# Optimization experiments

Hardware: AMD Instinct MI355X
Metric: run time of the kernel (lower is better)

The kernel has to match this reference:

```python
import jax, jax.numpy as jnp
import numpy as np

N_S, N_G, E = 4000, 50000, 250000   # sample nodes, gene nodes, edges per relation
D, H, C1, C3 = 128, 4, 32, 64       # input dim, heads, layer-1 per-head dim, layer-3 per-head dim
NEG_SLOPE = 0.2


def gatv2(x_src, x_dst, src, dst, ea, Wl, bl, Wr, br, We, att, bias, n_dst, concat):
    """PyG GATv2Conv (add_self_loops=False, edge_dim=1, eval mode)."""
    Hh, C = att.shape
    xl = (x_src @ Wl + bl).reshape(-1, Hh, C)          # [N_src, H, C]
    xr = (x_dst @ Wr + br).reshape(-1, Hh, C)          # [N_dst, H, C]
    ee = (ea @ We).reshape(-1, Hh, C)                  # [E, H, C]
    m = jax.nn.leaky_relu(xl[src] + xr[dst] + ee, NEG_SLOPE)   # [E, H, C]
    logits = jnp.einsum('ehc,hc->eh', m, att)          # [E, H]
    # segment softmax over incoming edges of each destination node
    lmax = jax.ops.segment_max(logits, dst, num_segments=n_dst)[dst]
    ex = jnp.exp(logits - lmax)
    denom = jax.ops.segment_sum(ex, dst, num_segments=n_dst)[dst]
    alpha = ex / denom                                 # [E, H]
    out = jax.ops.segment_sum(xl[src] * alpha[:, :, None], dst, num_segments=n_dst)  # [N_dst, H, C]
    out = out.reshape(n_dst, Hh * C) if concat else out.mean(axis=1)
    return out + bias


def setup_inputs() -> dict:
    key = jax.random.key(0)
    ks = jax.random.split(key, 40)
    p = lambda i, shape: jax.random.normal(ks[i], shape, dtype=jnp.float32) * 0.05
    HC1, HC3 = H * C1, H * C3
    inp = {
        'x_mrna': p(0, (N_S, D)),
        'x_gene': p(1, (N_G, D)),
        'sg_src': jax.random.randint(ks[2], (E,), 0, N_S),
        'sg_dst': jax.random.randint(ks[3], (E,), 0, N_G),
        'gs_src': jax.random.randint(ks[4], (E,), 0, N_G),
        'gs_dst': jax.random.randint(ks[5], (E,), 0, N_S),
        'ea_sg': p(6, (E, 1)),
        'ea_gs': p(7, (E, 1)),
        # layer-1 GATv2 params, relation mrna->gene
        'Wl1_sg': p(8, (D, HC1)), 'bl1_sg': p(9, (HC1,)),
        'Wr1_sg': p(10, (D, HC1)), 'br1_sg': p(11, (HC1,)),
        'We1_sg': p(12, (1, HC1)), 'att1_sg': p(13, (H, C1)), 'bo1_sg': p(14, (HC1,)),
        # layer-1 GATv2 params, relation gene->mrna
        'Wl1_gs': p(15, (D, HC1)), 'bl1_gs': p(16, (HC1,)),
        'Wr1_gs': p(17, (D, HC1)), 'br1_gs': p(18, (HC1,)),
        'We1_gs': p(19, (1, HC1)), 'att1_gs': p(20, (H, C1)), 'bo1_gs': p(21, (HC1,)),
        # layer-3 GATv2 params, relation gene->mrna (concat=False)
        'Wl3_gs': p(22, (HC1, HC3)), 'bl3_gs': p(23, (HC3,)),
        'Wr3_gs': p(24, (HC1, HC3)), 'br3_gs': p(25, (HC3,)),
        'We3_gs': p(26, (1, HC3)), 'att3_gs': p(27, (H, C3)), 'bo3_gs': p(28, (C3,)),
        # self-loop linears for omic ('mrna') nodes
        'Wsl1': p(29, (D, C1)), 'bsl1': p(30, (C1,)),
        'Wsl3': p(31, (HC1, C3)), 'bsl3': p(32, (C3,)),
    }
    return inp


def reference(x_mrna, x_gene, sg_src, sg_dst, gs_src, gs_dst, ea_sg, ea_gs,
              Wl1_sg, bl1_sg, Wr1_sg, br1_sg, We1_sg, att1_sg, bo1_sg,
              Wl1_gs, bl1_gs, Wr1_gs, br1_gs, We1_gs, att1_gs, bo1_gs,
              Wl3_gs, bl3_gs, Wr3_gs, br3_gs, We3_gs, att3_gs, bo3_gs,
              Wsl1, bsl1, Wsl3, bsl3):
    # ---- layer 1 (HeteroConv over both relations) ----
    x1_gene = gatv2(x_mrna, x_gene, sg_src, sg_dst, ea_sg,
                    Wl1_sg, bl1_sg, Wr1_sg, br1_sg, We1_sg, att1_sg, bo1_sg, N_G, True)
    x1_mrna = gatv2(x_gene, x_mrna, gs_src, gs_dst, ea_gs,
                    Wl1_gs, bl1_gs, Wr1_gs, br1_gs, We1_gs, att1_gs, bo1_gs, N_S, True)
    # self-loop linear on omic nodes, repeated across heads (repeat(1, heads))
    x1_mrna = x1_mrna + jnp.tile(x_mrna @ Wsl1 + bsl1, (1, H))
    x1_mrna = jax.nn.relu(x1_mrna)
    x1_gene = jax.nn.relu(x1_gene)
    # ---- three_layers=False: x2 = x1; layer 3 (concat=False, head mean) ----
    x3_mrna = gatv2(x1_gene, x1_mrna, gs_src, gs_dst, ea_gs,
                    Wl3_gs, bl3_gs, Wr3_gs, br3_gs, We3_gs, att3_gs, bo3_gs, N_S, False)
    x3_mrna = x3_mrna + (x1_mrna @ Wsl3 + bsl3)
    x3_mrna = jax.nn.relu(x3_mrna)
    # integrator=None, single omic view -> squeeze to [N_S, C3]
    return x3_mrna
```

## Files before the change

kernel.cpp:

```cpp
#include <hip/hip_runtime.h>
#include <cstdint>
#include <cstddef>

#define NS 4000
#define NG 50000
#define NE 250000
#define DIM 128
#define NDST_TOT (NG + NS)

typedef __bf16 bf16_t;
typedef bf16_t bf16x8 __attribute__((ext_vector_type(8)));
typedef bf16_t bf16x4 __attribute__((ext_vector_type(4)));
typedef bf16_t bf16x2 __attribute__((ext_vector_type(2)));
typedef float floatx4 __attribute__((ext_vector_type(4)));

#define HIST_B 977
#define WT_TOT 143360
#define XM_W 64000
#define XG_W 800000
#define PREP_B 3935
struct HPArgs {
  const int* sgd; const int* gsd;
  int* cnt; unsigned short* rank_sg; unsigned short* rank_gs;
  const float* W[8]; bf16_t* Wt[8]; int N[8]; int e0[8];
  const float* xm; bf16_t* xbm;
  const float* xg; bf16_t* xbg;
};

__global__ __launch_bounds__(256) void histprep(HPArgs a) {
  if (blockIdx.x < HIST_B) {
    int e = blockIdx.x * 256 + threadIdx.x;
    if (e < NE) {
      a.rank_sg[e] = (unsigned short)atomicAdd(a.cnt + a.sgd[e], 1);
      a.rank_gs[e] = (unsigned short)atomicAdd(a.cnt + NG + a.gsd[e], 1);
    }
  } else {
    int u = (blockIdx.x - HIST_B) * 256 + threadIdx.x;
    if (u < WT_TOT) {
      int c = 0;
#pragma unroll
      for (int i = 1; i < 8; i++) if (u >= a.e0[i]) c = i;
      int idx = u - a.e0[c];
      int N = a.N[c];
      int k = idx / N, n = idx - k * N;
      a.Wt[c][n * 128 + k] = (bf16_t)a.W[c][idx];
    } else if (u < WT_TOT + XM_W) {
      int j = (u - WT_TOT) * 8;
      float4 v0 = *reinterpret_cast<const float4*>(a.xm + j);
      float4 v1 = *reinterpret_cast<const float4*>(a.xm + j + 4);
      bf16x8 b;
      b[0] = (bf16_t)v0.x; b[1] = (bf16_t)v0.y; b[2] = (bf16_t)v0.z; b[3] = (bf16_t)v0.w;
      b[4] = (bf16_t)v1.x; b[5] = (bf16_t)v1.y; b[6] = (bf16_t)v1.z; b[7] = (bf16_t)v1.w;
      *reinterpret_cast<bf16x8*>(a.xbm + j) = b;
    } else {
      int j = (u - WT_TOT - XM_W) * 8;
      float4 v0 = *reinterpret_cast<const float4*>(a.xg + j);
      float4 v1 = *reinterpret_cast<const float4*>(a.xg + j + 4);
      bf16x8 b;
      b[0] = (bf16_t)v0.x; b[1] = (bf16_t)v0.y; b[2] = (bf16_t)v0.z; b[3] = (bf16_t)v0.w;
      b[4] = (bf16_t)v1.x; b[5] = (bf16_t)v1.y; b[6] = (bf16_t)v1.z; b[7] = (bf16_t)v1.w;
      *reinterpret_cast<bf16x8*>(a.xbg + j) = b;
    }
  }
}

__global__ __launch_bounds__(1024) void scan_fused(const int* __restrict__ cnt,
                                                   int* __restrict__ rp,
                                                   int* af, int n) {
  __shared__ int wsum[16];
  __shared__ int pfx_s;
  int i = blockIdx.x * 1024 + threadIdx.x;
  int lane = threadIdx.x & 63, w = threadIdx.x >> 6;
  int v = (i < n) ? cnt[i] : 0;
  int x = v;
#pragma unroll
  for (int off = 1; off < 64; off <<= 1) {
    int y = __shfl_up(x, off);
    if (lane >= off) x += y;
  }
  if (lane == 63) wsum[w] = x;
  __syncthreads();
  if (w == 0 && lane < 16) {
    int s = wsum[lane];
#pragma unroll
    for (int off = 1; off < 16; off <<= 1) {
      int y = __shfl_up(s, off);
      if (lane >= off) s += y;
    }
    wsum[lane] = s;
  }
  __syncthreads();
  int incl = x + (w ? wsum[w - 1] : 0);
  if (threadIdx.x == 0) atomicExch(af + blockIdx.x, wsum[15] + 1);
  if (w == 0) {
    int pred = 0;
    if (lane < (int)blockIdx.x) {
      int t;
      while ((t = atomicAdd(af + lane, 0)) == 0) { __builtin_amdgcn_s_sleep(8); }
      pred = t - 1;
    }
#pragma unroll
    for (int off = 32; off > 0; off >>= 1) pred += __shfl_down(pred, off);
    if (lane == 0) pfx_s = pred;
  }
  __syncthreads();
  if (i < n) rp[i] = incl - v + pfx_s;
  if (i == 0) rp[n] = 2 * NE;
}

#define SCAT_HALF 245
#define SCAT_B 490
struct SGArgs {
  const int* sgd; const int* gsd; const int* sgs; const int* gss;
  const float* easg; const float* eags;
  const int* rp; const unsigned short* rank_sg; const unsigned short* rank_gs;
  uint2* meta;
  const bf16_t* X[5];
  const bf16_t* Wt[5];
  const float* Bv[5];
  bf16_t* Y[5];
  int M[5];
  int Ncol[5];
  int blk0[5];
};

__global__ __launch_bounds__(256, 4) void scatgemm(SGArgs a) {
  if (blockIdx.x < SCAT_B) {
    int rel = (int)blockIdx.x >= SCAT_HALF;
    int b = (int)blockIdx.x - (rel ? SCAT_HALF : 0);
    int t4 = (b * 256 + (int)threadIdx.x) * 4;
    if (t4 < NE) {
      const int* dp = rel ? a.gsd : a.sgd;
      const int* sp = rel ? a.gss : a.sgs;
      const float* ep = rel ? a.eags : a.easg;
      const unsigned short* rk = rel ? a.rank_gs : a.rank_sg;
      const int* rpb = a.rp + (rel ? NG : 0);
      int4 d4 = *reinterpret_cast<const int4*>(dp + t4);
      int4 s4 = *reinterpret_cast<const int4*>(sp + t4);
      float4 e4 = *reinterpret_cast<const float4*>(ep + t4);
      ushort4 r4 = *reinterpret_cast<const ushort4*>(rk + t4);
      int p0 = rpb[d4.x] + (int)r4.x;
      int p1 = rpb[d4.y] + (int)r4.y;
      int p2 = rpb[d4.z] + (int)r4.z;
      int p3 = rpb[d4.w] + (int)r4.w;
      uint2 v0, v1, v2, v3;
      v0.x = (unsigned)s4.x; v0.y = __float_as_uint(e4.x);
      v1.x = (unsigned)s4.y; v1.y = __float_as_uint(e4.y);
      v2.x = (unsigned)s4.z; v2.y = __float_as_uint(e4.z);
      v3.x = (unsigned)s4.w; v3.y = __float_as_uint(e4.w);
      a.meta[p0] = v0;
      a.meta[p1] = v1;
      a.meta[p2] = v2;
      a.meta[p3] = v3;
    }
    return;
  }
  int bid = blockIdx.x - SCAT_B;
  int c = 0;
#pragma unroll
  for (int i = 1; i < 5; i++) if (bid >= a.blk0[i]) c = i;
  const bf16_t* X = a.X[c];
  const bf16_t* Wt = a.Wt[c];
  const float* B = a.Bv[c];
  bf16_t* Y = a.Y[c];
  int M = a.M[c];
  int N = a.Ncol[c];

  int wv = threadIdx.x >> 6, lane = threadIdx.x & 63;
  int m16 = lane & 15, quad = lane >> 4;
  int wrow0 = (bid - a.blk0[c]) * 256 + wv * 64;

  bf16x8 afrag[4][4];
#pragma unroll
  for (int rt = 0; rt < 4; rt++) {
    int arow = wrow0 + rt * 16 + m16;
    const bf16_t* xp = X + (size_t)arow * DIM + quad * 8;
#pragma unroll
    for (int kk = 0; kk < 4; kk++) {
      bf16x8 av = {};
      if (arow < M) av = *reinterpret_cast<const bf16x8*>(xp + kk * 32);
      afrag[rt][kk] = av;
    }
  }

  int ncols = N >> 4;
  for (int nt = 0; nt < ncols; nt++) {
    const bf16_t* bptr = Wt + (size_t)(nt * 16 + m16) * DIM + quad * 8;
    bf16x8 bfrag[4];
#pragma unroll
    for (int kk = 0; kk < 4; kk++)
      bfrag[kk] = *reinterpret_cast<const bf16x8*>(bptr + kk * 32);
    float4 bias = *reinterpret_cast<const float4*>(B + nt * 16 + quad * 4);
#pragma unroll
    for (int rt = 0; rt < 4; rt++) {
      floatx4 acc = {0.f, 0.f, 0.f, 0.f};
#pragma unroll
      for (int kk = 0; kk < 4; kk++)
        acc = __builtin_amdgcn_mfma_f32_16x16x32_bf16(bfrag[kk], afrag[rt][kk], acc, 0, 0, 0);
      int row = wrow0 + rt * 16 + m16;
      if (row < M) {
        bf16x4 o;
        o[0] = (bf16_t)(acc[0] + bias.x);
        o[1] = (bf16_t)(acc[1] + bias.y);
        o[2] = (bf16_t)(acc[2] + bias.z);
        o[3] = (bf16_t)(acc[3] + bias.w);
        *reinterpret_cast<bf16x4*>(Y + (size_t)row * N + nt * 16 + quad * 4) = o;
      }
    }
  }
}

template <int NCFG>
struct GArgs {
  const bf16_t* X[NCFG];
  const bf16_t* Wt[NCFG];
  const float* Bv[NCFG];
  bf16_t* Y[NCFG];
  int M[NCFG];
  int Ncol[NCFG];
  int blk0[NCFG];
};

template <int NCFG>
__global__ __launch_bounds__(256, 4) void gemm_multi(GArgs<NCFG> a) {
  int c = 0;
#pragma unroll
  for (int i = 1; i < NCFG; i++) if ((int)blockIdx.x >= a.blk0[i]) c = i;
  const bf16_t* X = a.X[c];
  const bf16_t* Wt = a.Wt[c];
  const float* B = a.Bv[c];
  bf16_t* Y = a.Y[c];
  int M = a.M[c];
  int N = a.Ncol[c];

  int wv = threadIdx.x >> 6, lane = threadIdx.x & 63;
  int m16 = lane & 15, quad = lane >> 4;
  int wrow0 = ((int)blockIdx.x - a.blk0[c]) * 128 + wv * 32;

  bf16x8 afrag[2][4];
#pragma unroll
  for (int rt = 0; rt < 2; rt++) {
    int arow = wrow0 + rt * 16 + m16;
    const bf16_t* xp = X + (size_t)arow * DIM + quad * 8;
#pragma unroll
    for (int kk = 0; kk < 4; kk++) {
      bf16x8 av = {};
      if (arow < M) av = *reinterpret_cast<const bf16x8*>(xp + kk * 32);
      afrag[rt][kk] = av;
    }
  }

  int ncols = N >> 4;
  for (int nt = 0; nt < ncols; nt++) {
    const bf16_t* bptr = Wt + (size_t)(nt * 16 + m16) * DIM + quad * 8;
    bf16x8 bfrag[4];
#pragma unroll
    for (int kk = 0; kk < 4; kk++)
      bfrag[kk] = *reinterpret_cast<const bf16x8*>(bptr + kk * 32);
    float4 bias = *reinterpret_cast<const float4*>(B + nt * 16 + quad * 4);
#pragma unroll
    for (int rt = 0; rt < 2; rt++) {
      floatx4 acc = {0.f, 0.f, 0.f, 0.f};
#pragma unroll
      for (int kk = 0; kk < 4; kk++)
        acc = __builtin_amdgcn_mfma_f32_16x16x32_bf16(bfrag[kk], afrag[rt][kk], acc, 0, 0, 0);
      int row = wrow0 + rt * 16 + m16;
      if (row < M) {
        bf16x4 o;
        o[0] = (bf16_t)(acc[0] + bias.x);
        o[1] = (bf16_t)(acc[1] + bias.y);
        o[2] = (bf16_t)(acc[2] + bias.z);
        o[3] = (bf16_t)(acc[3] + bias.w);
        *reinterpret_cast<bf16x4*>(Y + (size_t)row * N + nt * 16 + quad * 4) = o;
      }
    }
  }
}

#define SGB 3125
__global__ __launch_bounds__(256) void gatC(
    const int* __restrict__ rp, const uint2* __restrict__ meta,
    const float* __restrict__ WeS, const float* __restrict__ attS,
    const float* __restrict__ boS,
    const bf16_t* __restrict__ xlS, const bf16_t* __restrict__ xrS,
    bf16_t* __restrict__ outS,
    const float* __restrict__ WeG, const float* __restrict__ attG,
    const float* __restrict__ boG,
    const bf16_t* __restrict__ xlG, const bf16_t* __restrict__ xrG,
    const bf16_t* __restrict__ slG, bf16_t* __restrict__ outG) {
  __shared__ uint2 smeta[256];
  __shared__ float lacc[16][128];
  __shared__ float lden[16][4];
  int lane = threadIdx.x & 63, wv = threadIdx.x >> 6;
  int gl = lane & 15, grp = lane >> 4;

  if (blockIdx.x < SGB) {
    int wid = blockIdx.x * 4 + wv;
    int d0 = wid * 4;
    int q = lane < 5 ? lane : 0;
    int rv = rp[d0 + q];
    int beg = __shfl(rv, grp), end = __shfl(rv, grp + 1);
    int dst = d0 + grp;

    float wev[8], atv[8], xrv[8], acc[8];
    *reinterpret_cast<float4*>(wev) = *reinterpret_cast<const float4*>(WeS + gl * 8);
    *reinterpret_cast<float4*>(wev + 4) = *reinterpret_cast<const float4*>(WeS + gl * 8 + 4);
    *reinterpret_cast<float4*>(atv) = *reinterpret_cast<const float4*>(attS + gl * 8);
    *reinterpret_cast<float4*>(atv + 4) = *reinterpret_cast<const float4*>(attS + gl * 8 + 4);
    bf16x8 xrb = *reinterpret_cast<const bf16x8*>(xrS + (size_t)dst * 128 + gl * 8);
#pragma unroll
    for (int v = 0; v < 8; v++) { xrv[v] = (float)xrb[v]; acc[v] = 0.f; }
    float den = 0.f;

    for (int i0 = beg; i0 < end; i0 += 16) {
      int cnt = min(16, end - i0);
      int s_l = 0; float ea_l = 0.f;
      if (gl < cnt) {
        uint2 mv = meta[i0 + gl];
        s_l = (int)mv.x; ea_l = __uint_as_float(mv.y);
      }
      int base = lane & 48;
      float ea = __shfl(ea_l, base);
      bf16x8 xlb = *reinterpret_cast<const bf16x8*>(
          xlS + (size_t)__shfl(s_l, base) * 128 + gl * 8);
      for (int k = 0; k < cnt; k++) {
        bf16x8 cur = xlb;
        float eac = ea;
        if (k + 1 < cnt) {
          ea = __shfl(ea_l, base + k + 1);
          xlb = *reinterpret_cast<const bf16x8*>(
              xlS + (size_t)__shfl(s_l, base + k + 1) * 128 + gl * 8);
        }
        float p = 0.f, xf[8];
#pragma unroll
        for (int v = 0; v < 8; v++) {
          xf[v] = (float)cur[v];
          float z = fmaf(eac, wev[v], xrv[v]) + xf[v];
          z = z > 0.f ? z : 0.2f * z;
          p = fmaf(z, atv[v], p);
        }
        p += __shfl_xor(p, 1);
        p += __shfl_xor(p, 2);
        float ex = __expf(p);
        den += ex;
#pragma unroll
        for (int v = 0; v < 8; v++) acc[v] = fmaf(ex, xf[v], acc[v]);
      }
    }
    float inv = den > 0.f ? 1.f / den : 0.f;
    bf16x8 o;
#pragma unroll
    for (int v = 0; v < 8; v++) {
      float val = acc[v] * inv + boS[gl * 8 + v];
      o[v] = (bf16_t)(val > 0.f ? val : 0.f);
    }
    *reinterpret_cast<bf16x8*>(outS + (size_t)dst * 128 + gl * 8) = o;
  } else {
    int d = (int)blockIdx.x - SGB;
    const int* rpg = rp + NG;
    int G = wv * 4 + grp;
    int tid = threadIdx.x;

    float wev[8], atv[8], xrv[8], acc[8];
    *reinterpret_cast<float4*>(wev) = *reinterpret_cast<const float4*>(WeG + gl * 8);
    *reinterpret_cast<float4*>(wev + 4) = *reinterpret_cast<const float4*>(WeG + gl * 8 + 4);
    *reinterpret_cast<float4*>(atv) = *reinterpret_cast<const float4*>(attG + gl * 8);
    *reinterpret_cast<float4*>(atv + 4) = *reinterpret_cast<const float4*>(attG + gl * 8 + 4);
    bf16x8 xrb = *reinterpret_cast<const bf16x8*>(xrG + (size_t)d * 128 + gl * 8);
#pragma unroll
    for (int v = 0; v < 8; v++) { xrv[v] = (float)xrb[v]; acc[v] = 0.f; }
    float den = 0.f;

    int beg = rpg[d], end = rpg[d + 1];
    for (int base = beg; base < end; base += 256) {
      int cntb = min(256, end - base);
      __syncthreads();
      if (tid < cntb) smeta[tid] = meta[base + tid];
      __syncthreads();
      int e = G;
      uint2 mv; bf16x8 xlb;
      if (e < cntb) {
        mv = smeta[e];
        xlb = *reinterpret_cast<const bf16x8*>(xlG + (size_t)mv.x * 128 + gl * 8);
      }
      while (e < cntb) {
        bf16x8 cur = xlb;
        float eac = __uint_as_float(mv.y);
        int en = e + 16;
        if (en < cntb) {
          mv = smeta[en];
          xlb = *reinterpret_cast<const bf16x8*>(xlG + (size_t)mv.x * 128 + gl * 8);
        }
        float p = 0.f, xf[8];
#pragma unroll
        for (int v = 0; v < 8; v++) {
          xf[v] = (float)cur[v];
          float z = fmaf(eac, wev[v], xrv[v]) + xf[v];
          z = z > 0.f ? z : 0.2f * z;
          p = fmaf(z, atv[v], p);
        }
        p += __shfl_xor(p, 1);
        p += __shfl_xor(p, 2);
        float ex = __expf(p);
        den += ex;
#pragma unroll
        for (int v = 0; v < 8; v++) acc[v] = fmaf(ex, xf[v], acc[v]);
        e = en;
      }
    }
#pragma unroll
    for (int v = 0; v < 8; v++) lacc[G][gl * 8 + v] = acc[v];
    if ((gl & 3) == 0) lden[G][gl >> 2] = den;
    __syncthreads();
    if (wv != 0) return;
    int ch = lane * 2;
    int h = lane >> 4;
    float a0 = 0.f, a1 = 0.f, dh = 0.f;
#pragma unroll
    for (int g2 = 0; g2 < 16; g2++) {
      a0 += lacc[g2][ch];
      a1 += lacc[g2][ch + 1];
      dh += lden[g2][h];
    }
    float inv = dh > 0.f ? 1.f / dh : 0.f;
    float v0 = a0 * inv + boG[ch] + (float)slG[(size_t)d * 32 + (ch & 31)];
    float v1 = a1 * inv + boG[ch + 1] + (float)slG[(size_t)d * 32 + ((ch + 1) & 31)];
    bf16x2 o;
    o[0] = (bf16_t)(v0 > 0.f ? v0 : 0.f);
    o[1] = (bf16_t)(v1 > 0.f ? v1 : 0.f);
    *reinterpret_cast<bf16x2*>(outG + (size_t)d * 128 + ch) = o;
  }
}

__global__ __launch_bounds__(256) void gatE(
    const int* __restrict__ rp, const uint2* __restrict__ meta,
    const float* __restrict__ We, const float* __restrict__ att,
    const bf16_t* __restrict__ xl, const bf16_t* __restrict__ xr,
    const float* __restrict__ bo, const bf16_t* __restrict__ sl,
    float* __restrict__ out) {
  __shared__ uint2 smeta[256];
  __shared__ float lacc[16][256];
  __shared__ float lden[16][4];
  int lane = threadIdx.x & 63, wv = threadIdx.x >> 6;
  int gl = lane & 15, grp = lane >> 4;
  int G = wv * 4 + grp;
  int tid = threadIdx.x;
  int d = blockIdx.x;

  float wev[16], atv[16], xrv[16], acc[16];
#pragma unroll
  for (int b = 0; b < 4; b++) {
    *reinterpret_cast<float4*>(wev + b * 4) =
        *reinterpret_cast<const float4*>(We + gl * 16 + b * 4);
    *reinterpret_cast<float4*>(atv + b * 4) =
        *reinterpret_cast<const float4*>(att + gl * 16 + b * 4);
  }
  {
    bf16x8 r0 = *reinterpret_cast<const bf16x8*>(xr + (size_t)d * 256 + gl * 16);
    bf16x8 r1 = *reinterpret_cast<const bf16x8*>(xr + (size_t)d * 256 + gl * 16 + 8);
#pragma unroll
    for (int v = 0; v < 8; v++) { xrv[v] = (float)r0[v]; xrv[v + 8] = (float)r1[v]; }
  }
#pragma unroll
  for (int v = 0; v < 16; v++) acc[v] = 0.f;
  float den = 0.f;

  int beg = rp[d], end = rp[d + 1];
  for (int base = beg; base < end; base += 256) {
    int cntb = min(256, end - base);
    __syncthreads();
    if (tid < cntb) smeta[tid] = meta[base + tid];
    __syncthreads();
    int e = G;
    uint2 mv; bf16x8 x0, x1;
    if (e < cntb) {
      mv = smeta[e];
      x0 = *reinterpret_cast<const bf16x8*>(xl + (size_t)mv.x * 256 + gl * 16);
      x1 = *reinterpret_cast<const bf16x8*>(xl + (size_t)mv.x * 256 + gl * 16 + 8);
    }
    while (e < cntb) {
      bf16x8 c0 = x0, c1 = x1;
      float eac = __uint_as_float(mv.y);
      int en = e + 16;
      if (en < cntb) {
        mv = smeta[en];
        x0 = *reinterpret_cast<const bf16x8*>(xl + (size_t)mv.x * 256 + gl * 16);
        x1 = *reinterpret_cast<const bf16x8*>(xl + (size_t)mv.x * 256 + gl * 16 + 8);
      }
      float p = 0.f, xf[16];
#pragma unroll
      for (int v = 0; v < 8; v++) { xf[v] = (float)c0[v]; xf[v + 8] = (float)c1[v]; }
#pragma unroll
      for (int v = 0; v < 16; v++) {
        float z = fmaf(eac, wev[v], xrv[v]) + xf[v];
        z = z > 0.f ? z : 0.2f * z;
        p = fmaf(z, atv[v], p);
      }
      p += __shfl_xor(p, 1);
      p += __shfl_xor(p, 2);
      float ex = __expf(p);
      den += ex;
#pragma unroll
      for (int v = 0; v < 16; v++) acc[v] = fmaf(ex, xf[v], acc[v]);
      e = en;
    }
  }
#pragma unroll
  for (int v = 0; v < 16; v++) lacc[G][gl * 16 + v] = acc[v];
  if ((gl & 3) == 0) lden[G][gl >> 2] = den;
  __syncthreads();
  if (wv != 0) return;
  int ch = lane * 4;
  int h = lane >> 4;
  float a[4] = {0.f, 0.f, 0.f, 0.f};
  float dh = 0.f;
#pragma unroll
  for (int g2 = 0; g2 < 16; g2++) {
#pragma unroll
    for (int v = 0; v < 4; v++) a[v] += lacc[g2][ch + v];
    dh += lden[g2][h];
  }
  float inv = dh > 0.f ? 1.f / dh : 0.f;
#pragma unroll
  for (int v = 0; v < 4; v++) {
    float s_ = a[v] * inv;
    s_ += __shfl_xor(s_, 16);
    s_ += __shfl_xor(s_, 32);
    if (lane < 16) {
      int c = (lane & 15) * 4 + v;
      float val = 0.25f * s_ + bo[c] + (float)sl[(size_t)d * 64 + c];
      out[(size_t)d * 64 + c] = val > 0.f ? val : 0.f;
    }
  }
}


static inline int nblk(long long threads) { return (int)((threads + 255) / 256); }
static inline int nrow(int M, int R) { return (M + R - 1) / R; }

extern "C" void kernel_launch(void* const* d_in, const int* in_sizes, int n_in,
                              void* d_out, int out_size, void* d_ws, size_t ws_size,
                              hipStream_t stream) {
  const float* x_mrna = (const float*)d_in[0];
  const float* x_gene = (const float*)d_in[1];
  const int* sg_src = (const int*)d_in[2];
  const int* sg_dst = (const int*)d_in[3];
  const int* gs_src = (const int*)d_in[4];
  const int* gs_dst = (const int*)d_in[5];
  const float* ea_sg = (const float*)d_in[6];
  const float* ea_gs = (const float*)d_in[7];
  const float* Wl1_sg = (const float*)d_in[8];
  const float* bl1_sg = (const float*)d_in[9];
  const float* Wr1_sg = (const float*)d_in[10];
  const float* br1_sg = (const float*)d_in[11];
  const float* We1_sg = (const float*)d_in[12];
  const float* att1_sg = (const float*)d_in[13];
  const float* bo1_sg = (const float*)d_in[14];
  const float* Wl1_gs = (const float*)d_in[15];
  const float* bl1_gs = (const float*)d_in[16];
  const float* Wr1_gs = (const float*)d_in[17];
  const float* br1_gs = (const float*)d_in[18];
  const float* We1_gs = (const float*)d_in[19];
  const float* att1_gs = (const float*)d_in[20];
  const float* bo1_gs = (const float*)d_in[21];
  const float* Wl3_gs = (const float*)d_in[22];
  const float* bl3_gs = (const float*)d_in[23];
  const float* Wr3_gs = (const float*)d_in[24];
  const float* br3_gs = (const float*)d_in[25];
  const float* We3_gs = (const float*)d_in[26];
  const float* att3_gs = (const float*)d_in[27];
  const float* bo3_gs = (const float*)d_in[28];
  const float* Wsl1 = (const float*)d_in[29];
  const float* bsl1 = (const float*)d_in[30];
  const float* Wsl3 = (const float*)d_in[31];
  const float* bsl3 = (const float*)d_in[32];

  float* ws = (float*)d_ws;
  bf16_t* xl1_gs = (bf16_t*)(ws + 0);
  bf16_t* xl1_sg = (bf16_t*)(ws + 3200000);
  bf16_t* xr1_sg = (bf16_t*)(ws + 3456000);
  bf16_t* xr1_gs = (bf16_t*)(ws + 6656000);
  bf16_t* xl3    = (bf16_t*)(ws + 0);
  bf16_t* xr3    = (bf16_t*)(ws + 6400000);
  bf16_t* xb_mrna = (bf16_t*)(ws + 6912000);
  bf16_t* xb_gene = (bf16_t*)(ws + 7168000);
  bf16_t* x1_gene = (bf16_t*)(ws + 10368000);
  bf16_t* x1_mrna = (bf16_t*)(ws + 13568000);
  bf16_t* sl1    = (bf16_t*)(ws + 13824000);
  bf16_t* sl3    = (bf16_t*)(ws + 13856000);
  int*   ib      = (int*)(ws + 13920000);
  int* cnt  = ib + 0;
  int* af   = ib + 54000;
  int* rpc  = ib + 54064;
  unsigned short* rank_sg = (unsigned short*)(ib + 108066);
  unsigned short* rank_gs = (unsigned short*)(ib + 233066);
  uint2* meta = (uint2*)(ib + 358066);
  bf16_t* wtb = (bf16_t*)(ib + 1358066);

  bf16_t* wt_l1sg = wtb + 0;
  bf16_t* wt_r1sg = wtb + 16384;
  bf16_t* wt_l1gs = wtb + 32768;
  bf16_t* wt_r1gs = wtb + 49152;
  bf16_t* wt_l3   = wtb + 65536;
  bf16_t* wt_r3   = wtb + 98304;
  bf16_t* wt_sl1  = wtb + 131072;
  bf16_t* wt_sl3  = wtb + 135168;

  hipMemsetAsync(cnt, 0, (54000 + 64) * sizeof(int), stream);

  {
    HPArgs hp;
    hp.sgd = sg_dst; hp.gsd = gs_dst;
    hp.cnt = cnt; hp.rank_sg = rank_sg; hp.rank_gs = rank_gs;
    const float* Wsrc[8] = {Wl1_sg, Wr1_sg, Wl1_gs, Wr1_gs, Wl3_gs, Wr3_gs, Wsl1, Wsl3};
    bf16_t* Wdst[8] = {wt_l1sg, wt_r1sg, wt_l1gs, wt_r1gs, wt_l3, wt_r3, wt_sl1, wt_sl3};
    int Nn[8] = {128, 128, 128, 128, 256, 256, 32, 64};
    int e0[8] = {0, 16384, 32768, 49152, 65536, 98304, 131072, 135168};
    for (int i = 0; i < 8; i++) { hp.W[i] = Wsrc[i]; hp.Wt[i] = Wdst[i]; hp.N[i] = Nn[i]; hp.e0[i] = e0[i]; }
    hp.xm = x_mrna; hp.xbm = xb_mrna;
    hp.xg = x_gene; hp.xbg = xb_gene;
    histprep<<<HIST_B + PREP_B, 256, 0, stream>>>(hp);
  }

  int nchunks = (NDST_TOT + 1023) / 1024;
  scan_fused<<<nchunks, 1024, 0, stream>>>(cnt, rpc, af, NDST_TOT);

  {
    SGArgs sa;
    sa.sgd = sg_dst; sa.gsd = gs_dst; sa.sgs = sg_src; sa.gss = gs_src;
    sa.easg = ea_sg; sa.eags = ea_gs;
    sa.rp = rpc; sa.rank_sg = rank_sg; sa.rank_gs = rank_gs; sa.meta = meta;
    const bf16_t* Xs[5] = {xb_mrna, xb_gene, xb_gene, xb_mrna, xb_mrna};
    const bf16_t* Ws[5] = {wt_l1sg, wt_r1sg, wt_l1gs, wt_r1gs, wt_sl1};
    const float* Bs[5] = {bl1_sg, br1_sg, bl1_gs, br1_gs, bsl1};
    bf16_t* Ys[5] = {xl1_sg, xr1_sg, xl1_gs, xr1_gs, sl1};
    int Ms[5] = {NS, NG, NG, NS, NS};
    int Ns[5] = {128, 128, 128, 128, 32};
    int b0 = 0;
    for (int i = 0; i < 5; i++) {
      sa.X[i] = Xs[i]; sa.Wt[i] = Ws[i]; sa.Bv[i] = Bs[i]; sa.Y[i] = Ys[i];
      sa.M[i] = Ms[i]; sa.Ncol[i] = Ns[i]; sa.blk0[i] = b0;
      b0 += nrow(Ms[i], 256);
    }
    scatgemm<<<SCAT_B + b0, 256, 0, stream>>>(sa);
  }

  gatC<<<SGB + NS, 256, 0, stream>>>(
      rpc, meta,
      We1_sg, att1_sg, bo1_sg, xl1_sg, xr1_sg, x1_gene,
      We1_gs, att1_gs, bo1_gs, xl1_gs, xr1_gs, sl1, x1_mrna);

  {
    GArgs<3> ga;
    const bf16_t* Xs[3] = {x1_gene, x1_mrna, x1_mrna};
    const bf16_t* Ws[3] = {wt_l3, wt_r3, wt_sl3};
    const float* Bs[3] = {bl3_gs, br3_gs, bsl3};
    bf16_t* Ys[3] = {xl3, xr3, sl3};
    int Ms[3] = {NG, NS, NS};
    int Ns[3] = {256, 256, 64};
    int b0 = 0;
    for (int i = 0; i < 3; i++) {
      ga.X[i] = Xs[i]; ga.Wt[i] = Ws[i]; ga.Bv[i] = Bs[i]; ga.Y[i] = Ys[i];
      ga.M[i] = Ms[i]; ga.Ncol[i] = Ns[i]; ga.blk0[i] = b0;
      b0 += nrow(Ms[i], 128);
    }
    gemm_multi<3><<<b0, 256, 0, stream>>>(ga);
  }

  gatE<<<NS, 256, 0, stream>>>(rpc + NG, meta, We3_gs, att3_gs,
                               xl3, xr3, bo3_gs, sl3, (float*)d_out);
}
```

Before: 279.2 us.

## Regroup preprocessing: pair histogram with layer-1 GEMM, run scatter standalone

Restructures the pre-attention pipeline. A standalone prep kernel now does the bf16 conversion and weight transposes. The edge histogram atomics are fused into the layer-1 GEMM launch, placed after the GEMM blocks, and the CSR scatter becomes its own kernel after the scan. The intent is to overlap the atomic-heavy histogram with MFMA GEMM work instead of with the conversion pass. The cost is one extra kernel launch and a scatter that no longer overlaps with anything.

Result: no change. 279.3 us (+0.0%).

```diff
diff --git a/kernel.cpp b/kernel.cpp
--- a/kernel.cpp
+++ b/kernel.cpp
@@ -14,107 +14,50 @@
 typedef bf16_t bf16x2 __attribute__((ext_vector_type(2)));
 typedef float floatx4 __attribute__((ext_vector_type(4)));
 
-#define HIST_B 977
 #define WT_TOT 143360
 #define XM_W 64000
 #define XG_W 800000
 #define PREP_B 3935
-struct HPArgs {
-  const int* sgd; const int* gsd;
-  int* cnt; unsigned short* rank_sg; unsigned short* rank_gs;
+struct PArgs {
   const float* W[8]; bf16_t* Wt[8]; int N[8]; int e0[8];
   const float* xm; bf16_t* xbm;
   const float* xg; bf16_t* xbg;
 };
 
-__global__ __launch_bounds__(256) void histprep(HPArgs a) {
-  if (blockIdx.x < HIST_B) {
-    int e = blockIdx.x * 256 + threadIdx.x;
-    if (e < NE) {
-      a.rank_sg[e] = (unsigned short)atomicAdd(a.cnt + a.sgd[e], 1);
-      a.rank_gs[e] = (unsigned short)atomicAdd(a.cnt + NG + a.gsd[e], 1);
-    }
+__global__ __launch_bounds__(256) void prep(PArgs a) {
+  int u = blockIdx.x * 256 + threadIdx.x;
+  if (u < WT_TOT) {
+    int c = 0;
+#pragma unroll
+    for (int i = 1; i < 8; i++) if (u >= a.e0[i]) c = i;
+    int idx = u - a.e0[c];
+    int N = a.N[c];
+    int k = idx / N, n = idx - k * N;
+    a.Wt[c][n * 128 + k] = (bf16_t)a.W[c][idx];
+  } else if (u < WT_TOT + XM_W) {
+    int j = (u - WT_TOT) * 8;
+    float4 v0 = *reinterpret_cast<const float4*>(a.xm + j);
+    float4 v1 = *reinterpret_cast<const float4*>(a.xm + j + 4);
+    bf16x8 b;
+    b[0] = (bf16_t)v0.x; b[1] = (bf16_t)v0.y; b[2] = (bf16_t)v0.z; b[3] = (bf16_t)v0.w;
+    b[4] = (bf16_t)v1.x; b[5] = (bf16_t)v1.y; b[6] = (bf16_t)v1.z; b[7] = (bf16_t)v1.w;
+    *reinterpret_cast<bf16x8*>(a.xbm + j) = b;
   } else {
-    int u = (blockIdx.x - HIST_B) * 256 + threadIdx.x;
-    if (u < WT_TOT) {
-      int c = 0;
-#pragma unroll
-      for (int i = 1; i < 8; i++) if (u >= a.e0[i]) c = i;
-      int idx = u - a.e0[c];
-      int N = a.N[c];
-      int k = idx / N, n = idx - k * N;
-      a.Wt[c][n * 128 + k] = (bf16_t)a.W[c][idx];
-    } else if (u < WT_TOT + XM_W) {
-      int j = (u - WT_TOT) * 8;
-      float4 v0 = *reinterpret_cast<const float4*>(a.xm + j);
-      float4 v1 = *reinterpret_cast<const float4*>(a.xm + j + 4);
-      bf16x8 b;
-      b[0] = (bf16_t)v0.x; b[1] = (bf16_t)v0.y; b[2] = (bf16_t)v0.z; b[3] = (bf16_t)v0.w;
-      b[4] = (bf16_t)v1.x; b[5] = (bf16_t)v1.y; b[6] = (bf16_t)v1.z; b[7] = (bf16_t)v1.w;
-      *reinterpret_cast<bf16x8*>(a.xbm + j) = b;
-    } else {
-      int j = (u - WT_TOT - XM_W) * 8;
-      float4 v0 = *reinterpret_cast<const float4*>(a.xg + j);
-      float4 v1 = *reinterpret_cast<const float4*>(a.xg + j + 4);
-      bf16x8 b;
-      b[0] = (bf16_t)v0.x; b[1] = (bf16_t)v0.y; b[2] = (bf16_t)v0.z; b[3] = (bf16_t)v0.w;
-      b[4] = (bf16_t)v1.x; b[5] = (bf16_t)v1.y; b[6] = (bf16_t)v1.z; b[7] = (bf16_t)v1.w;
-      *reinterpret_cast<bf16x8*>(a.xbg + j) = b;
-    }
-  }
-}
-
-__global__ __launch_bounds__(1024) void scan_fused(const int* __restrict__ cnt,
-                                                   int* __restrict__ rp,
-                                                   int* af, int n) {
-  __shared__ int wsum[16];
-  __shared__ int pfx_s;
-  int i = blockIdx.x * 1024 + threadIdx.x;
-  int lane = threadIdx.x & 63, w = threadIdx.x >> 6;
-  int v = (i < n) ? cnt[i] : 0;
-  int x = v;
-#pragma unroll
-  for (int off = 1; off < 64; off <<= 1) {
-    int y = __shfl_up(x, off);
-    if (lane >= off) x += y;
-  }
-  if (lane == 63) wsum[w] = x;
-  __syncthreads();
-  if (w == 0 && lane < 16) {
-    int s = wsum[lane];
-#pragma unroll
-    for (int off = 1; off < 16; off <<= 1) {
-      int y = __shfl_up(s, off);
-      if (lane >= off) s += y;
-    }
-    wsum[lane] = s;
-  }
-  __syncthreads();
-  int incl = x + (w ? wsum[w - 1] : 0);
-  if (threadIdx.x == 0) atomicExch(af + blockIdx.x, wsum[15] + 1);
-  if (w == 0) {
-    int pred = 0;
-    if (lane < (int)blockIdx.x) {
-      int t;
-      while ((t = atomicAdd(af + lane, 0)) == 0) { __builtin_amdgcn_s_sleep(8); }
-      pred = t - 1;
-    }
-#pragma unroll
-    for (int off = 32; off > 0; off >>= 1) pred += __shfl_down(pred, off);
-    if (lane == 0) pfx_s = pred;
-  }
-  __syncthreads();
-  if (i < n) rp[i] = incl - v + pfx_s;
-  if (i == 0) rp[n] = 2 * NE;
-}
-
-#define SCAT_HALF 245
-#define SCAT_B 490
-struct SGArgs {
-  const int* sgd; const int* gsd; const int* sgs; const int* gss;
-  const float* easg; const float* eags;
-  const int* rp; const unsigned short* rank_sg; const unsigned short* rank_gs;
-  uint2* meta;
+    int j = (u - WT_TOT - XM_W) * 8;
+    float4 v0 = *reinterpret_cast<const float4*>(a.xg + j);
+    float4 v1 = *reinterpret_cast<const float4*>(a.xg + j + 4);
+    bf16x8 b;
+    b[0] = (bf16_t)v0.x; b[1] = (bf16_t)v0.y; b[2] = (bf16_t)v0.z; b[3] = (bf16_t)v0.w;
+    b[4] = (bf16_t)v1.x; b[5] = (bf16_t)v1.y; b[6] = (bf16_t)v1.z; b[7] = (bf16_t)v1.w;
+    *reinterpret_cast<bf16x8*>(a.xbg + j) = b;
+  }
+}
+
+#define HIST_B 977
+struct HGArgs {
+  const int* sgd; const int* gsd;
+  int* cnt; unsigned short* rank_sg; unsigned short* rank_gs;
+  int hist0;
   const bf16_t* X[5];
   const bf16_t* Wt[5];
   const float* Bv[5];
@@ -124,38 +67,16 @@
   int blk0[5];
 };
 
-__global__ __launch_bounds__(256, 4) void scatgemm(SGArgs a) {
-  if (blockIdx.x < SCAT_B) {
-    int rel = (int)blockIdx.x >= SCAT_HALF;
-    int b = (int)blockIdx.x - (rel ? SCAT_HALF : 0);
-    int t4 = (b * 256 + (int)threadIdx.x) * 4;
-    if (t4 < NE) {
-      const int* dp = rel ? a.gsd : a.sgd;
-      const int* sp = rel ? a.gss : a.sgs;
-      const float* ep = rel ? a.eags : a.easg;
-      const unsigned short* rk = rel ? a.rank_gs : a.rank_sg;
-      const int* rpb = a.rp + (rel ? NG : 0);
-      int4 d4 = *reinterpret_cast<const int4*>(dp + t4);
-      int4 s4 = *reinterpret_cast<const int4*>(sp + t4);
-      float4 e4 = *reinterpret_cast<const float4*>(ep + t4);
-      ushort4 r4 = *reinterpret_cast<const ushort4*>(rk + t4);
-      int p0 = rpb[d4.x] + (int)r4.x;
-      int p1 = rpb[d4.y] + (int)r4.y;
-      int p2 = rpb[d4.z] + (int)r4.z;
-      int p3 = rpb[d4.w] + (int)r4.w;
-      uint2 v0, v1, v2, v3;
-      v0.x = (unsigned)s4.x; v0.y = __float_as_uint(e4.x);
-      v1.x = (unsigned)s4.y; v1.y = __float_as_uint(e4.y);
-      v2.x = (unsigned)s4.z; v2.y = __float_as_uint(e4.z);
-      v3.x = (unsigned)s4.w; v3.y = __float_as_uint(e4.w);
-      a.meta[p0] = v0;
-      a.meta[p1] = v1;
-      a.meta[p2] = v2;
-      a.meta[p3] = v3;
+__global__ __launch_bounds__(256, 4) void histgemm(HGArgs a) {
+  if ((int)blockIdx.x >= a.hist0) {
+    int e = ((int)blockIdx.x - a.hist0) * 256 + threadIdx.x;
+    if (e < NE) {
+      a.rank_sg[e] = (unsigned short)atomicAdd(a.cnt + a.sgd[e], 1);
+      a.rank_gs[e] = (unsigned short)atomicAdd(a.cnt + NG + a.gsd[e], 1);
     }
     return;
   }
-  int bid = blockIdx.x - SCAT_B;
+  int bid = blockIdx.x;
   int c = 0;
 #pragma unroll
   for (int i = 1; i < 5; i++) if (bid >= a.blk0[i]) c = i;
@@ -207,6 +128,89 @@
         *reinterpret_cast<bf16x4*>(Y + (size_t)row * N + nt * 16 + quad * 4) = o;
       }
     }
+  }
+}
+
+__global__ __launch_bounds__(1024) void scan_fused(const int* __restrict__ cnt,
+                                                   int* __restrict__ rp,
+                                                   int* af, int n) {
+  __shared__ int wsum[16];
+  __shared__ int pfx_s;
+  int i = blockIdx.x * 1024 + threadIdx.x;
+  int lane = threadIdx.x & 63, w = threadIdx.x >> 6;
+  int v = (i < n) ? cnt[i] : 0;
+  int x = v;
+#pragma unroll
+  for (int off = 1; off < 64; off <<= 1) {
+    int y = __shfl_up(x, off);
+    if (lane >= off) x += y;
+  }
+  if (lane == 63) wsum[w] = x;
+  __syncthreads();
+  if (w == 0 && lane < 16) {
+    int s = wsum[lane];
+#pragma unroll
+    for (int off = 1; off < 16; off <<= 1) {
+      int y = __shfl_up(s, off);
+      if (lane >= off) s += y;
+    }
+    wsum[lane] = s;
+  }
+  __syncthreads();
+  int incl = x + (w ? wsum[w - 1] : 0);
+  if (threadIdx.x == 0) atomicExch(af + blockIdx.x, wsum[15] + 1);
+  if (w == 0) {
+    int pred = 0;
+    if (lane < (int)blockIdx.x) {
+      int t;
+      while ((t = atomicAdd(af + lane, 0)) == 0) { __builtin_amdgcn_s_sleep(8); }
+      pred = t - 1;
+    }
+#pragma unroll
+    for (int off = 32; off > 0; off >>= 1) pred += __shfl_down(pred, off);
+    if (lane == 0) pfx_s = pred;
+  }
+  __syncthreads();
+  if (i < n) rp[i] = incl - v + pfx_s;
+  if (i == 0) rp[n] = 2 * NE;
+}
+
+#define SCAT_HALF 245
+#define SCAT_B 490
+struct ScArgs {
+  const int* sgd; const int* gsd; const int* sgs; const int* gss;
+  const float* easg; const float* eags;
+  const int* rp; const unsigned short* rank_sg; const unsigned short* rank_gs;
+  uint2* meta;
+};
+
+__global__ __launch_bounds__(256) void scat(ScArgs a) {
+  int rel = (int)blockIdx.x >= SCAT_HALF;
+  int b = (int)blockIdx.x - (rel ? SCAT_HALF : 0);
+  int t4 = (b * 256 + (int)threadIdx.x) * 4;
+  if (t4 < NE) {
+    const int* dp = rel ? a.gsd : a.sgd;
+    const int* sp = rel ? a.gss : a.sgs;
+    const float* ep = rel ? a.eags : a.easg;
+    const unsigned short* rk = rel ? a.rank_gs : a.rank_sg;
+    const int* rpb = a.rp + (rel ? NG : 0);
+    int4 d4 = *reinterpret_cast<const int4*>(dp + t4);
+    int4 s4 = *reinterpret_cast<const int4*>(sp + t4);
+    float4 e4 = *reinterpret_cast<const float4*>(ep + t4);
+    ushort4 r4 = *reinterpret_cast<const ushort4*>(rk + t4);
+    int p0 = rpb[d4.x] + (int)r4.x;
+    int p1 = rpb[d4.y] + (int)r4.y;
+    int p2 = rpb[d4.z] + (int)r4.z;
+    int p3 = rpb[d4.w] + (int)r4.w;
+    uint2 v0, v1, v2, v3;
+    v0.x = (unsigned)s4.x; v0.y = __float_as_uint(e4.x);
+    v1.x = (unsigned)s4.y; v1.y = __float_as_uint(e4.y);
+    v2.x = (unsigned)s4.z; v2.y = __float_as_uint(e4.z);
+    v3.x = (unsigned)s4.w; v3.y = __float_as_uint(e4.w);
+    a.meta[p0] = v0;
+    a.meta[p1] = v1;
+    a.meta[p2] = v2;
+    a.meta[p3] = v3;
   }
 }
 
@@ -609,27 +613,21 @@
   hipMemsetAsync(cnt, 0, (54000 + 64) * sizeof(int), stream);
 
   {
-    HPArgs hp;
-    hp.sgd = sg_dst; hp.gsd = gs_dst;
-    hp.cnt = cnt; hp.rank_sg = rank_sg; hp.rank_gs = rank_gs;
+    PArgs pa;
     const float* Wsrc[8] = {Wl1_sg, Wr1_sg, Wl1_gs, Wr1_gs, Wl3_gs, Wr3_gs, Wsl1, Wsl3};
     bf16_t* Wdst[8] = {wt_l1sg, wt_r1sg, wt_l1gs, wt_r1gs, wt_l3, wt_r3, wt_sl1, wt_sl3};
     int Nn[8] = {128, 128, 128, 128, 256, 256, 32, 64};
     int e0[8] = {0, 16384, 32768, 49152, 65536, 98304, 131072, 135168};
-    for (int i = 0; i < 8; i++) { hp.W[i] = Wsrc[i]; hp.Wt[i] = Wdst[i]; hp.N[i] = Nn[i]; hp.e0[i] = e0[i]; }
-    hp.xm = x_mrna; hp.xbm = xb_mrna;
-    hp.xg = x_gene; hp.xbg = xb_gene;
-    histprep<<<HIST_B + PREP_B, 256, 0, stream>>>(hp);
-  }
-
-  int nchunks = (NDST_TOT + 1023) / 1024;
-  scan_fused<<<nchunks, 1024, 0, stream>>>(cnt, rpc, af, NDST_TOT);
+    for (int i = 0; i < 8; i++) { pa.W[i] = Wsrc[i]; pa.Wt[i] = Wdst[i]; pa.N[i] = Nn[i]; pa.e0[i] = e0[i]; }
+    pa.xm = x_mrna; pa.xbm = xb_mrna;
+    pa.xg = x_gene; pa.xbg = xb_gene;
+    prep<<<PREP_B, 256, 0, stream>>>(pa);
+  }
 
   {
-    SGArgs sa;
-    sa.sgd = sg_dst; sa.gsd = gs_dst; sa.sgs = sg_src; sa.gss = gs_src;
-    sa.easg = ea_sg; sa.eags = ea_gs;
-    sa.rp = rpc; sa.rank_sg = rank_sg; sa.rank_gs = rank_gs; sa.meta = meta;
+    HGArgs hg;
+    hg.sgd = sg_dst; hg.gsd = gs_dst;
+    hg.cnt = cnt; hg.rank_sg = rank_sg; hg.rank_gs = rank_gs;
     const bf16_t* Xs[5] = {xb_mrna, xb_gene, xb_gene, xb_mrna, xb_mrna};
     const bf16_t* Ws[5] = {wt_l1sg, wt_r1sg, wt_l1gs, wt_r1gs, wt_sl1};
     const float* Bs[5] = {bl1_sg, br1_sg, bl1_gs, br1_gs, bsl1};
@@ -638,11 +636,23 @@
     int Ns[5] = {128, 128, 128, 128, 32};
     int b0 = 0;
     for (int i = 0; i < 5; i++) {
-      sa.X[i] = Xs[i]; sa.Wt[i] = Ws[i]; sa.Bv[i] = Bs[i]; sa.Y[i] = Ys[i];
-      sa.M[i] = Ms[i]; sa.Ncol[i] = Ns[i]; sa.blk0[i] = b0;
+      hg.X[i] = Xs[i]; hg.Wt[i] = Ws[i]; hg.Bv[i] = Bs[i]; hg.Y[i] = Ys[i];
+      hg.M[i] = Ms[i]; hg.Ncol[i] = Ns[i]; hg.blk0[i] = b0;
       b0 += nrow(Ms[i], 256);
     }
-    scatgemm<<<SCAT_B + b0, 256, 0, stream>>>(sa);
+    hg.hist0 = b0;
+    histgemm<<<b0 + HIST_B, 256, 0, stream>>>(hg);
+  }
+
+  int nchunks = (NDST_TOT + 1023) / 1024;
+  scan_fused<<<nchunks, 1024, 0, stream>>>(cnt, rpc, af, NDST_TOT);
+
+  {
+    ScArgs sa;
+    sa.sgd = sg_dst; sa.gsd = gs_dst; sa.sgs = sg_src; sa.gss = gs_src;
+    sa.easg = ea_sg; sa.eags = ea_gs;
+    sa.rp = rpc; sa.rank_sg = rank_sg; sa.rank_gs = rank_gs; sa.meta = meta;
+    scat<<<SCAT_B, 256, 0, stream>>>(sa);
   }
 
   gatC<<<SGB + NS, 256, 0, stream>>>(
```
